# Kernel tuning notes

Measured on AMD Instinct MI355X. Metric: run time of the kernel, lower is better.

## Reference

```python
import jax, jax.numpy as jnp
import numpy as np

NUM_EXPERTS = 16
TOP_K = 2
D_IN = 1024
D_HID = 4096
D_OUT = 1024
BATCH = 8192


def setup_inputs() -> dict:
    key = jax.random.key(0)
    ks = jax.random.split(key, 6)
    s_in = 1.0 / np.sqrt(D_IN)
    s_hid = 1.0 / np.sqrt(D_HID)
    return {
        "x": jax.random.normal(ks[0], (BATCH, D_IN), dtype=jnp.float32),
        "Wg": jax.random.normal(ks[1], (D_IN, NUM_EXPERTS), dtype=jnp.float32) * s_in,
        "W1": jax.random.normal(ks[2], (NUM_EXPERTS, D_IN, D_HID), dtype=jnp.float32) * s_in,
        "b1": jnp.zeros((NUM_EXPERTS, D_HID), dtype=jnp.float32),
        "W2": jax.random.normal(ks[3], (NUM_EXPERTS, D_HID, D_OUT), dtype=jnp.float32) * s_hid,
        "b2": jnp.zeros((NUM_EXPERTS, D_OUT), dtype=jnp.float32),
    }


def _moe_forward(x, Wg, W1, b1, W2, b2):
    # Gating: top-k routing with softmax over the selected logits.
    logits = x @ Wg                                   # [B, E]
    top_vals, top_idx = jax.lax.top_k(logits, TOP_K)  # [B, k]
    routing_weights = jax.nn.softmax(top_vals, axis=-1)  # [B, k]

    # Per-token combine weight for each expert (sum over k slots):
    # cw[b, e] = sum_k routing_weights[b, k] * (top_idx[b, k] == e)
    one_hot = jax.nn.one_hot(top_idx, NUM_EXPERTS, dtype=x.dtype)  # [B, k, E]
    combine_w = jnp.einsum("bk,bke->be", routing_weights, one_hot)  # [B, E]

    # Per-expert MLP compute + weighted scatter-add combine.
    # Fixed-size loop over experts (structurally distinct weight slices);
    # equivalent math to the original's gather/compute/scatter dispatch.
    out = jnp.zeros((x.shape[0], D_OUT), dtype=x.dtype)
    for e in range(NUM_EXPERTS):
        h = jax.nn.relu(x @ W1[e] + b1[e])            # [B, H]
        y = h @ W2[e] + b2[e]                         # [B, O]
        out = out + combine_w[:, e:e + 1] * y
    return out


def reference(x, Wg, W1, b1, W2, b2):
    return _moe_forward(x, Wg, W1, b1, W2, b2)
```

## Files before the change

### kernel.cpp

```cpp
#include <hip/hip_runtime.h>
#include <cstdio>

#define DIN   1024
#define DHID  4096
#define DOUT  1024
#define NEXP  16
#define NTOK  8192
#define NPAIR (NTOK * 2)
#define PADMAX 18432
#define MAXTILES 144

typedef _Float16 h8 __attribute__((ext_vector_type(8)));
typedef _Float16 h4 __attribute__((ext_vector_type(4)));
typedef float    f4 __attribute__((ext_vector_type(4)));

#define C_CNT  0
#define C_POFF 16
#define C_CUR  32
#define C_NT   48
#define C_TE   64
#define C_TP   256

__device__ __forceinline__ void async16(const void* g, void* l) {
  __builtin_amdgcn_global_load_lds((const __attribute__((address_space(1))) void*)g,
                                   (__attribute__((address_space(3))) void*)l, 16, 0, 0);
}

__global__ void k_init(float* __restrict__ out, const float* __restrict__ x,
                       _Float16* __restrict__ x16, int* __restrict__ ptok,
                       float* __restrict__ pw, int* __restrict__ ctrl) {
  int i = blockIdx.x * 256 + threadIdx.x;
  ((f4*)out)[i] = (f4){0.f, 0.f, 0.f, 0.f};
  float4 v = ((const float4*)x)[i];
  h4 hv = {(_Float16)v.x, (_Float16)v.y, (_Float16)v.z, (_Float16)v.w};
  ((h4*)x16)[i] = hv;
  if (i < PADMAX) { ptok[i] = 0; pw[i] = 0.f; }
  if (i < 1024) ctrl[i] = 0;
}

__global__ void k_gate(const float* __restrict__ x, const float* __restrict__ wg,
                       int* __restrict__ te, float* __restrict__ tw,
                       int* __restrict__ ctrl) {
  int t = blockIdx.x * 4 + (threadIdx.x >> 6);
  int l = threadIdx.x & 63;
  const float* xr = x + (long)t * DIN;
  float acc[NEXP];
#pragma unroll
  for (int e = 0; e < NEXP; ++e) acc[e] = 0.f;
  for (int k = l; k < DIN; k += 64) {
    float xv = xr[k];
    const float4* wr = (const float4*)(wg + (long)k * NEXP);
    float4 a = wr[0], b = wr[1], c = wr[2], d = wr[3];
    acc[0]  += xv * a.x; acc[1]  += xv * a.y; acc[2]  += xv * a.z; acc[3]  += xv * a.w;
    acc[4]  += xv * b.x; acc[5]  += xv * b.y; acc[6]  += xv * b.z; acc[7]  += xv * b.w;
    acc[8]  += xv * c.x; acc[9]  += xv * c.y; acc[10] += xv * c.z; acc[11] += xv * c.w;
    acc[12] += xv * d.x; acc[13] += xv * d.y; acc[14] += xv * d.z; acc[15] += xv * d.w;
  }
#pragma unroll
  for (int off = 32; off > 0; off >>= 1) {
#pragma unroll
    for (int e = 0; e < NEXP; ++e) acc[e] += __shfl_xor(acc[e], off, 64);
  }
  if (l == 0) {
    float v0 = -1e30f; int e0 = 0;
#pragma unroll
    for (int e = 0; e < NEXP; ++e) if (acc[e] > v0) { v0 = acc[e]; e0 = e; }
    float v1 = -1e30f; int e1 = 0;
#pragma unroll
    for (int e = 0; e < NEXP; ++e) if (e != e0 && acc[e] > v1) { v1 = acc[e]; e1 = e; }
    float d = expf(v1 - v0);
    float den = 1.f / (1.f + d);
    te[2 * t] = e0;     tw[2 * t] = den;
    te[2 * t + 1] = e1; tw[2 * t + 1] = d * den;
    atomicAdd(&ctrl[C_CNT + e0], 1);
    atomicAdd(&ctrl[C_CNT + e1], 1);
  }
}

__global__ void k_scan(int* __restrict__ ctrl) {
  __shared__ int sOff[NEXP], sT0[NEXP], sTiles[NEXP];
  int tid = threadIdx.x;
  if (tid == 0) {
    int off = 0, nt = 0;
    for (int e = 0; e < NEXP; ++e) {
      int c = ctrl[C_CNT + e];
      int tiles = (c + 127) >> 7;
      ctrl[C_POFF + e] = off;
      ctrl[C_CUR + e] = off;
      sOff[e] = off; sT0[e] = nt; sTiles[e] = tiles;
      nt += tiles;
      off += tiles * 128;
    }
    ctrl[C_NT] = nt;
  }
  __syncthreads();
  int nt = sT0[NEXP - 1] + sTiles[NEXP - 1];
  for (int j = tid; j < nt; j += blockDim.x) {
    int e = 0;
#pragma unroll
    for (int k = 1; k < NEXP; ++k) if (j >= sT0[k]) e = k;
    ctrl[C_TE + j] = e;
    ctrl[C_TP + j] = sOff[e] + (j - sT0[e]) * 128;
  }
}

__global__ void k_assign(const int* __restrict__ te, const float* __restrict__ tw,
                         int* __restrict__ ctrl, int* __restrict__ ptok,
                         float* __restrict__ pw) {
  int t = blockIdx.x * 256 + threadIdx.x;
#pragma unroll
  for (int s = 0; s < 2; ++s) {
    int e = te[2 * t + s];
    int pos = atomicAdd(&ctrl[C_CUR + e], 1);
    ptok[pos] = t;
    pw[pos] = tw[2 * t + s];
  }
}

__global__ void k_transpose(const float* __restrict__ W, _Float16* __restrict__ out,
                            int R, int C) {
  __shared__ __align__(16) _Float16 tile[64][136];
  int e = blockIdx.z;
  const float* Wb = W + ((long)e * R + blockIdx.x * 128) * C + blockIdx.y * 64;
  int tid = threadIdx.x;
  int rr = tid >> 4;
  int cc = (tid & 15) * 4;
#pragma unroll
  for (int i = 0; i < 8; ++i) {
    int r = rr + i * 16;
    float4 v = *(const float4*)(Wb + (long)r * C + cc);
    tile[cc + 0][r] = (_Float16)v.x;
    tile[cc + 1][r] = (_Float16)v.y;
    tile[cc + 2][r] = (_Float16)v.z;
    tile[cc + 3][r] = (_Float16)v.w;
  }
  __syncthreads();
  _Float16* ob = out + ((long)e * C + blockIdx.y * 64) * R + blockIdx.x * 128;
  int c2 = tid >> 4;
  int ch = tid & 15;
#pragma unroll
  for (int i = 0; i < 4; ++i) {
    int c = c2 + i * 16;
    *(h8*)(ob + (long)c * R + ch * 8) = *(const h8*)&tile[c][ch * 8];
  }
}

template<int KD, int ND, int G1>
__global__ __launch_bounds__(256)
void k_gemm(const _Float16* __restrict__ A, const _Float16* __restrict__ Wt,
            const float* __restrict__ bias, const int* __restrict__ ctrl,
            const int* __restrict__ ptok, const float* __restrict__ pw,
            _Float16* __restrict__ Hout, float* __restrict__ out) {
  __shared__ __align__(16) _Float16 sm[32768];
  _Float16* As0 = sm;
  _Float16* Bs0 = sm + 8192;
  _Float16* As1 = sm + 16384;
  _Float16* Bs1 = sm + 24576;

  int mt = blockIdx.y;
  if (mt >= ctrl[C_NT]) return;
  int e  = ctrl[C_TE + mt];
  int p0 = ctrl[C_TP + mt];
  int n0 = blockIdx.x * 128;
  int tid = threadIdx.x;
  int w = tid >> 6, l = tid & 63;
  int wm = w & 1, wn = w >> 1;
  int ln15 = l & 15, lq = l >> 4;

  const _Float16* ag[4];
  const _Float16* bg[4];
#pragma unroll
  for (int j = 0; j < 4; ++j) {
    int r = (w * 4 + j) * 8 + (l >> 3);
    int c = (l & 7) ^ (r & 7);
    long arow = G1 ? (long)ptok[p0 + r] : (long)(p0 + r);
    ag[j] = A + arow * KD + c * 8;
    bg[j] = Wt + ((long)e * ND + n0 + r) * KD + c * 8;
  }

  f4 acc[4][4];
#pragma unroll
  for (int i = 0; i < 4; ++i)
#pragma unroll
    for (int j = 0; j < 4; ++j) acc[i][j] = (f4){0.f, 0.f, 0.f, 0.f};

  auto stage = [&](int k0, _Float16* A_, _Float16* B_) {
#pragma unroll
    for (int j = 0; j < 4; ++j) {
      async16(ag[j] + k0, A_ + (w * 4 + j) * 512);
      async16(bg[j] + k0, B_ + (w * 4 + j) * 512);
    }
  };
  auto compute = [&](const _Float16* A_, const _Float16* B_) {
#pragma unroll
    for (int ks = 0; ks < 2; ++ks) {
      h8 af[4], bf[4];
      int kq = ks * 4 + lq;
#pragma unroll
      for (int i = 0; i < 4; ++i) {
        int m = wm * 64 + i * 16 + ln15;
        af[i] = *(const h8*)&A_[m * 64 + (kq ^ (m & 7)) * 8];
      }
#pragma unroll
      for (int j = 0; j < 4; ++j) {
        int n = wn * 64 + j * 16 + ln15;
        bf[j] = *(const h8*)&B_[n * 64 + (kq ^ (n & 7)) * 8];
      }
#pragma unroll
      for (int i = 0; i < 4; ++i)
#pragma unroll
        for (int j = 0; j < 4; ++j)
          acc[i][j] = __builtin_amdgcn_mfma_f32_16x16x32_f16(af[i], bf[j], acc[i][j], 0, 0, 0);
    }
  };

  constexpr int KSTEPS = KD / 64;
  stage(0, As0, Bs0);
  __syncthreads();
#pragma unroll 1
  for (int t = 0; t < KSTEPS; t += 2) {
    stage((t + 1) * 64, As1, Bs1);
    compute(As0, Bs0);
    __syncthreads();
    if (t + 2 < KSTEPS) stage((t + 2) * 64, As0, Bs0);
    compute(As1, Bs1);
    __syncthreads();
  }

  float bj[4];
#pragma unroll
  for (int j = 0; j < 4; ++j) bj[j] = bias[e * ND + n0 + wn * 64 + j * 16 + ln15];

  if (G1) {
#pragma unroll
    for (int i = 0; i < 4; ++i)
#pragma unroll
      for (int reg = 0; reg < 4; ++reg) {
        int row = wm * 64 + i * 16 + lq * 4 + reg;
#pragma unroll
        for (int j = 0; j < 4; ++j)
          sm[row * 136 + wn * 64 + j * 16 + ln15] =
              (_Float16)fmaxf(acc[i][j][reg] + bj[j], 0.f);
      }
    __syncthreads();
#pragma unroll
    for (int p = 0; p < 8; ++p) {
      int idx = p * 256 + tid;
      int row = idx >> 4, ch = idx & 15;
      *(h8*)(Hout + (long)(p0 + row) * DHID + n0 + ch * 8) =
          *(const h8*)&sm[row * 136 + ch * 8];
    }
  } else {
#pragma unroll
    for (int i = 0; i < 4; ++i)
#pragma unroll
      for (int reg = 0; reg < 4; ++reg) {
        int p = p0 + wm * 64 + i * 16 + lq * 4 + reg;
        float wgt = pw[p];
        if (wgt != 0.f) {
          int t = ptok[p];
          float* orow = out + (long)t * DOUT + n0 + wn * 64 + ln15;
#pragma unroll
          for (int j = 0; j < 4; ++j)
            atomicAdd(&orow[j * 16], wgt * (acc[i][j][reg] + bj[j]));
        }
      }
  }
}

extern "C" void kernel_launch(void* const* d_in, const int* in_sizes, int n_in,
                              void* d_out, int out_size, void* d_ws, size_t ws_size,
                              hipStream_t stream) {
  const float* x  = (const float*)d_in[0];
  const float* Wg = (const float*)d_in[1];
  const float* W1 = (const float*)d_in[2];
  const float* b1 = (const float*)d_in[3];
  const float* W2 = (const float*)d_in[4];
  const float* b2 = (const float*)d_in[5];
  float* out = (float*)d_out;
  char* ws = (char*)d_ws;

  size_t WT_OFF = 0;
  size_t H_OFF  = WT_OFF + (size_t)NEXP * DHID * DIN * 2;
  size_t X_OFF  = H_OFF  + (size_t)PADMAX * DHID * 2;
  size_t TE_OFF = X_OFF  + (size_t)NTOK * DIN * 2;
  size_t TW_OFF = TE_OFF + (size_t)NPAIR * 4;
  size_t PT_OFF = TW_OFF + (size_t)NPAIR * 4;
  size_t PW_OFF = PT_OFF + (size_t)PADMAX * 4;
  size_t CT_OFF = PW_OFF + (size_t)PADMAX * 4;
  size_t END    = CT_OFF + 4096;
  if (ws_size < END) {
    fprintf(stderr, "kernel_launch: ws too small (%zu < %zu)\n", ws_size, END);
    return;
  }
  _Float16* Wt  = (_Float16*)(ws + WT_OFF);
  _Float16* H   = (_Float16*)(ws + H_OFF);
  _Float16* x16 = (_Float16*)(ws + X_OFF);
  int*   te   = (int*)(ws + TE_OFF);
  float* tw   = (float*)(ws + TW_OFF);
  int*   pt   = (int*)(ws + PT_OFF);
  float* pw   = (float*)(ws + PW_OFF);
  int*   ctrl = (int*)(ws + CT_OFF);

  k_init<<<NTOK * DIN / (256 * 4), 256, 0, stream>>>(out, x, x16, pt, pw, ctrl);
  k_gate<<<NTOK / 4, 256, 0, stream>>>(x, Wg, te, tw, ctrl);
  k_scan<<<1, 256, 0, stream>>>(ctrl);
  k_assign<<<NTOK / 256, 256, 0, stream>>>(te, tw, ctrl, pt, pw);

  k_transpose<<<dim3(DIN / 128, DHID / 64, NEXP), 256, 0, stream>>>(W1, Wt, DIN, DHID);
  k_gemm<DIN, DHID, 1><<<dim3(DHID / 128, MAXTILES), 256, 0, stream>>>(
      x16, Wt, b1, ctrl, pt, pw, H, nullptr);

  k_transpose<<<dim3(DHID / 128, DOUT / 64, NEXP), 256, 0, stream>>>(W2, Wt, DHID, DOUT);
  k_gemm<DHID, DOUT, 0><<<dim3(DOUT / 128, MAXTILES), 256, 0, stream>>>(
      H, Wt, b2, ctrl, pt, pw, nullptr, out);
}
```

Measured before the change: 1.307 ms.

## Repack expert weights into k-octet-major fp16 layout and remap GEMM grid across XCDs

Replaces the shared-memory transpose with a grid-stride kernel that casts weights to fp16 in a [e][k/8][n][8] layout, so each 16-byte chunk holds eight consecutive k values for one output column and the GEMM B loads index it directly. The GEMM grid is flattened to one dimension and the block id is permuted so consecutive tiles are grouped per XCD (bid & 7), aiming for better L2 reuse of shared weight and activation tiles. MFMA sections are wrapped with s_setprio to favour the matrix issue. The new weight-prep kernel reads strided fp32 columns with no shared-memory staging, which could coalesce worse than the old transpose.

```diff
diff --git a/kernel.cpp b/kernel.cpp
--- a/kernel.cpp
+++ b/kernel.cpp
@@ -117,31 +117,20 @@
   }
 }
 
-__global__ void k_transpose(const float* __restrict__ W, _Float16* __restrict__ out,
-                            int R, int C) {
-  __shared__ __align__(16) _Float16 tile[64][136];
-  int e = blockIdx.z;
-  const float* Wb = W + ((long)e * R + blockIdx.x * 128) * C + blockIdx.y * 64;
-  int tid = threadIdx.x;
-  int rr = tid >> 4;
-  int cc = (tid & 15) * 4;
-#pragma unroll
-  for (int i = 0; i < 8; ++i) {
-    int r = rr + i * 16;
-    float4 v = *(const float4*)(Wb + (long)r * C + cc);
-    tile[cc + 0][r] = (_Float16)v.x;
-    tile[cc + 1][r] = (_Float16)v.y;
-    tile[cc + 2][r] = (_Float16)v.z;
-    tile[cc + 3][r] = (_Float16)v.w;
-  }
-  __syncthreads();
-  _Float16* ob = out + ((long)e * C + blockIdx.y * 64) * R + blockIdx.x * 128;
-  int c2 = tid >> 4;
-  int ch = tid & 15;
-#pragma unroll
-  for (int i = 0; i < 4; ++i) {
-    int c = c2 + i * 16;
-    *(h8*)(ob + (long)c * R + ch * 8) = *(const h8*)&tile[c][ch * 8];
+__global__ void k_wprep(const float* __restrict__ W, _Float16* __restrict__ Wt,
+                        int KD, int ND) {
+  int KO = KD >> 3;
+  long total = (long)NEXP * KO * ND;
+  long stride = (long)gridDim.x * blockDim.x;
+  for (long it = (long)blockIdx.x * blockDim.x + threadIdx.x; it < total; it += stride) {
+    long n  = it & (ND - 1);
+    long ko = (it / ND) & (KO - 1);
+    long e  = it / ((long)ND * KO);
+    const float* src = W + (e * KD + ko * 8) * ND + n;
+    h8 v;
+#pragma unroll
+    for (int kk = 0; kk < 8; ++kk) v[kk] = (_Float16)src[(long)kk * ND];
+    *(h8*)(Wt + it * 8) = v;
   }
 }
 
@@ -152,46 +141,56 @@
             const int* __restrict__ ptok, const float* __restrict__ pw,
             _Float16* __restrict__ Hout, float* __restrict__ out) {
   __shared__ __align__(16) _Float16 sm[32768];
-  _Float16* As0 = sm;
-  _Float16* Bs0 = sm + 8192;
-  _Float16* As1 = sm + 16384;
-  _Float16* Bs1 = sm + 24576;
-
-  int mt = blockIdx.y;
+
+  constexpr int NB = ND / 128;
+  constexpr int KO = KD / 8;
+  constexpr int NW = NB * MAXTILES;
+  constexpr int QX = NW / 8;
+  int bid = blockIdx.x;
+  int wid = (bid & 7) * QX + (bid >> 3);
+  int nb = wid % NB;
+  int mt = wid / NB;
+
   if (mt >= ctrl[C_NT]) return;
   int e  = ctrl[C_TE + mt];
   int p0 = ctrl[C_TP + mt];
-  int n0 = blockIdx.x * 128;
+  int n0 = nb * 128;
   int tid = threadIdx.x;
   int w = tid >> 6, l = tid & 63;
   int wm = w & 1, wn = w >> 1;
   int ln15 = l & 15, lq = l >> 4;
 
-  const _Float16* ag[4];
-  const _Float16* bg[4];
+  long aoff[4], boff[4];
 #pragma unroll
   for (int j = 0; j < 4; ++j) {
     int r = (w * 4 + j) * 8 + (l >> 3);
     int c = (l & 7) ^ (r & 7);
     long arow = G1 ? (long)ptok[p0 + r] : (long)(p0 + r);
-    ag[j] = A + arow * KD + c * 8;
-    bg[j] = Wt + ((long)e * ND + n0 + r) * KD + c * 8;
-  }
-
-  f4 acc[4][4];
-#pragma unroll
-  for (int i = 0; i < 4; ++i)
-#pragma unroll
-    for (int j = 0; j < 4; ++j) acc[i][j] = (f4){0.f, 0.f, 0.f, 0.f};
-
-  auto stage = [&](int k0, _Float16* A_, _Float16* B_) {
+    aoff[j] = arow * KD + c * 8;
+    boff[j] = ((long)(e * KO + c) * ND + (n0 + r)) * 8;
+  }
+
+  auto stage = [&](int t, int d) {
+    _Float16* As = sm + d * 16384;
+    _Float16* Bs = As + 8192;
+    long ka = (long)t * 64;
+    long kb = (long)t * 64 * ND;
 #pragma unroll
     for (int j = 0; j < 4; ++j) {
-      async16(ag[j] + k0, A_ + (w * 4 + j) * 512);
-      async16(bg[j] + k0, B_ + (w * 4 + j) * 512);
+      async16(A + aoff[j] + ka, As + (w * 4 + j) * 512);
+      async16(Wt + boff[j] + kb, Bs + (w * 4 + j) * 512);
     }
   };
-  auto compute = [&](const _Float16* A_, const _Float16* B_) {
+
+  f4 acc[4][4];
+#pragma unroll
+  for (int i = 0; i < 4; ++i)
+#pragma unroll
+    for (int j = 0; j < 4; ++j) acc[i][j] = (f4){0.f, 0.f, 0.f, 0.f};
+
+  auto compute = [&](int d) {
+    const _Float16* As = sm + d * 16384;
+    const _Float16* Bs = As + 8192;
 #pragma unroll
     for (int ks = 0; ks < 2; ++ks) {
       h8 af[4], bf[4];
@@ -199,31 +198,34 @@
 #pragma unroll
       for (int i = 0; i < 4; ++i) {
         int m = wm * 64 + i * 16 + ln15;
-        af[i] = *(const h8*)&A_[m * 64 + (kq ^ (m & 7)) * 8];
+        af[i] = *(const h8*)&As[m * 64 + (kq ^ (m & 7)) * 8];
       }
 #pragma unroll
       for (int j = 0; j < 4; ++j) {
         int n = wn * 64 + j * 16 + ln15;
-        bf[j] = *(const h8*)&B_[n * 64 + (kq ^ (n & 7)) * 8];
+        bf[j] = *(const h8*)&Bs[n * 64 + (kq ^ (n & 7)) * 8];
       }
+      __builtin_amdgcn_s_setprio(1);
 #pragma unroll
       for (int i = 0; i < 4; ++i)
 #pragma unroll
         for (int j = 0; j < 4; ++j)
           acc[i][j] = __builtin_amdgcn_mfma_f32_16x16x32_f16(af[i], bf[j], acc[i][j], 0, 0, 0);
+      __builtin_amdgcn_s_setprio(0);
     }
   };
 
   constexpr int KSTEPS = KD / 64;
-  stage(0, As0, Bs0);
+
+  stage(0, 0);
   __syncthreads();
 #pragma unroll 1
   for (int t = 0; t < KSTEPS; t += 2) {
-    stage((t + 1) * 64, As1, Bs1);
-    compute(As0, Bs0);
+    stage(t + 1, 1);
+    compute(0);
     __syncthreads();
-    if (t + 2 < KSTEPS) stage((t + 2) * 64, As0, Bs0);
-    compute(As1, Bs1);
+    if (t + 2 < KSTEPS) stage(t + 2, 0);
+    compute(1);
     __syncthreads();
   }
 
@@ -232,6 +234,7 @@
   for (int j = 0; j < 4; ++j) bj[j] = bias[e * ND + n0 + wn * 64 + j * 16 + ln15];
 
   if (G1) {
+    _Float16* cs = sm;
 #pragma unroll
     for (int i = 0; i < 4; ++i)
 #pragma unroll
@@ -239,7 +242,7 @@
         int row = wm * 64 + i * 16 + lq * 4 + reg;
 #pragma unroll
         for (int j = 0; j < 4; ++j)
-          sm[row * 136 + wn * 64 + j * 16 + ln15] =
+          cs[row * 136 + wn * 64 + j * 16 + ln15] =
               (_Float16)fmaxf(acc[i][j][reg] + bj[j], 0.f);
       }
     __syncthreads();
@@ -248,7 +251,7 @@
       int idx = p * 256 + tid;
       int row = idx >> 4, ch = idx & 15;
       *(h8*)(Hout + (long)(p0 + row) * DHID + n0 + ch * 8) =
-          *(const h8*)&sm[row * 136 + ch * 8];
+          *(const h8*)&cs[row * 136 + ch * 8];
     }
   } else {
 #pragma unroll
@@ -258,8 +261,8 @@
         int p = p0 + wm * 64 + i * 16 + lq * 4 + reg;
         float wgt = pw[p];
         if (wgt != 0.f) {
-          int t = ptok[p];
-          float* orow = out + (long)t * DOUT + n0 + wn * 64 + ln15;
+          int tk = ptok[p];
+          float* orow = out + (long)tk * DOUT + n0 + wn * 64 + ln15;
 #pragma unroll
           for (int j = 0; j < 4; ++j)
             atomicAdd(&orow[j * 16], wgt * (acc[i][j][reg] + bj[j]));
@@ -307,11 +310,11 @@
   k_scan<<<1, 256, 0, stream>>>(ctrl);
   k_assign<<<NTOK / 256, 256, 0, stream>>>(te, tw, ctrl, pt, pw);
 
-  k_transpose<<<dim3(DIN / 128, DHID / 64, NEXP), 256, 0, stream>>>(W1, Wt, DIN, DHID);
-  k_gemm<DIN, DHID, 1><<<dim3(DHID / 128, MAXTILES), 256, 0, stream>>>(
+  k_wprep<<<4096, 256, 0, stream>>>(W1, Wt, DIN, DHID);
+  k_gemm<DIN, DHID, 1><<<dim3((DHID / 128) * MAXTILES), 256, 0, stream>>>(
       x16, Wt, b1, ctrl, pt, pw, H, nullptr);
 
-  k_transpose<<<dim3(DHID / 128, DOUT / 64, NEXP), 256, 0, stream>>>(W2, Wt, DHID, DOUT);
-  k_gemm<DHID, DOUT, 0><<<dim3(DOUT / 128, MAXTILES), 256, 0, stream>>>(
+  k_wprep<<<4096, 256, 0, stream>>>(W2, Wt, DHID, DOUT);
+  k_gemm<DHID, DOUT, 0><<<dim3((DOUT / 128) * MAXTILES), 256, 0, stream>>>(
       H, Wt, b2, ctrl, pt, pw, nullptr, out);
 }
```

New measurement: 1.345 ms. 1.03x slower.
